# Optimization experiments

Hardware: AMD Instinct MI355X
Metric: run time of the kernel (lower is better)

Reference implementation:

```python
import jax, jax.numpy as jnp
import numpy as np

ALPHA = 0.5
E_MINUS_1 = float(np.e - 1.0)  # exp(1) - 1; exp(0) - 1 == 0

B = 4096
CLASSES = [128, 512, 2048, 8192]


def _ce(logits, labels):
    # mean cross-entropy: -mean(log_softmax(logits)[i, labels[i]])
    logp = jax.nn.log_softmax(logits, axis=-1)
    nll = -jnp.take_along_axis(logp, labels[:, None], axis=-1)[:, 0]
    return jnp.mean(nll)


def setup_inputs() -> dict:
    key = jax.random.key(0)
    ks = jax.random.split(key, 12)
    inp = {}
    for l, c in enumerate(CLASSES):
        inp[f"out{l}"] = jax.random.normal(ks[l], (B, c), dtype=jnp.float32)
    # targets[:, l] must be < CLASSES[l]; keep all < min(CLASSES) for simplicity
    inp["targets"] = jax.random.randint(ks[4], (B, 4), 0, 128).astype(jnp.int64)
    for l, c in enumerate(CLASSES):
        inp[f"pred{l}"] = jax.random.randint(ks[5 + l], (B,), 0, c).astype(jnp.int64)
    inp["valid01"] = jax.random.randint(ks[9], (128, 512), 0, 2).astype(bool)
    inp["valid12"] = jax.random.randint(ks[10], (512, 2048), 0, 2).astype(bool)
    inp["valid23"] = jax.random.randint(ks[11], (2048, 8192), 0, 2).astype(bool)
    return inp


def reference(out0, out1, out2, out3, targets, pred0, pred1, pred2, pred3,
              valid01, valid12, valid23):
    outputs = [out0, out1, out2, out3]
    preds = [pred0, pred1, pred2, pred3]
    valids = [valid01, valid12, valid23]

    total_ce = sum(_ce(outputs[l], targets[:, l]) for l in range(len(outputs)))

    # dependency loss: per sample, exp(D)-1 with D=0 if (prev_pred -> curr_pred)
    # is a valid parent-child pair, else D=1; averaged over batch, summed over levels
    total_dep = jnp.zeros((), dtype=out0.dtype)
    for l, V in enumerate(valids):
        ok = V[preds[l], preds[l + 1]]  # [B] bool gather (vectorized dict lookup)
        total_dep = total_dep + E_MINUS_1 * jnp.mean(1.0 - ok.astype(out0.dtype))

    total = ALPHA * total_ce + (1.0 - ALPHA) * total_dep
    return (total, total_ce, total_dep)
```

## Files before the change

### kernel.cpp

```cpp
#include <hip/hip_runtime.h>
#include <float.h>


#define NB 4096

static constexpr float LOG2E = 1.4426950408889634f;
static constexpr float LN2   = 0.6931471805599453f;
static constexpr float E_M1  = 1.7182818284590452f;

__device__ __forceinline__ void combine_ms(float& m, float& s, float m2, float s2) {
    float mn = fmaxf(m, m2);
    s = s * exp2f((m - mn) * LOG2E) + s2 * exp2f((m2 - mn) * LOG2E);
    m = mn;
}

__global__ __launch_bounds__(256) void ce_rows_kernel(
    const float* __restrict__ o0, const float* __restrict__ o1,
    const float* __restrict__ o2, const float* __restrict__ o3,
    const int* __restrict__ targets, float* __restrict__ nll)
{
    const int bid = blockIdx.x;
    const int lvl = 3 - (bid >> 12);
    const int row = bid & (NB - 1);

    const float* base; int C;
    if      (lvl == 0) { base = o0; C = 128;  }
    else if (lvl == 1) { base = o1; C = 512;  }
    else if (lvl == 2) { base = o2; C = 2048; }
    else               { base = o3; C = 8192; }

    const float4* rowp = (const float4*)(base + (size_t)row * C);
    const int C4 = C >> 2;

    float m = -FLT_MAX, s = 0.0f;
    for (int f = threadIdx.x; f < C4; f += 256) {
        float4 v = rowp[f];
        float m4 = fmaxf(fmaxf(v.x, v.y), fmaxf(v.z, v.w));
        float mn = fmaxf(m, m4);
        s = s * exp2f((m - mn) * LOG2E)
          + exp2f((v.x - mn) * LOG2E) + exp2f((v.y - mn) * LOG2E)
          + exp2f((v.z - mn) * LOG2E) + exp2f((v.w - mn) * LOG2E);
        m = mn;
    }

    #pragma unroll
    for (int off = 32; off; off >>= 1)
        combine_ms(m, s, __shfl_xor(m, off), __shfl_xor(s, off));

    __shared__ float lm[4], ls[4];
    const int wv = threadIdx.x >> 6;
    if ((threadIdx.x & 63) == 0) { lm[wv] = m; ls[wv] = s; }
    __syncthreads();

    if (threadIdx.x == 0) {
        float M = lm[0], S = ls[0];
        #pragma unroll
        for (int w = 1; w < 4; w++) combine_ms(M, S, lm[w], ls[w]);
        const int t  = targets[row * 4 + lvl];
        const float xt = base[(size_t)row * C + t];
        nll[lvl * NB + row] = M + log2f(S) * LN2 - xt;
    }
}

__global__ __launch_bounds__(1024) void finalize_kernel(
    const float* __restrict__ nll,
    const int* __restrict__ p0, const int* __restrict__ p1,
    const int* __restrict__ p2, const int* __restrict__ p3,
    const int* __restrict__ v01, const int* __restrict__ v12,
    const int* __restrict__ v23, float* __restrict__ out)
{
    const int tid = threadIdx.x;

    float ce[4] = {0.f, 0.f, 0.f, 0.f};
    #pragma unroll
    for (int l = 0; l < 4; l++)
        for (int i = tid; i < NB; i += 1024)
            ce[l] += nll[l * NB + i];

    float ok[3] = {0.f, 0.f, 0.f};
    for (int i = tid; i < NB; i += 1024) {
        const int a = p0[i], b = p1[i], c = p2[i], d = p3[i];
        ok[0] += (v01[a * 512  + b] != 0) ? 1.f : 0.f;
        ok[1] += (v12[b * 2048 + c] != 0) ? 1.f : 0.f;
        ok[2] += (v23[c * 8192 + d] != 0) ? 1.f : 0.f;
    }

    __shared__ float lds[16];
    float vals[7] = {ce[0], ce[1], ce[2], ce[3], ok[0], ok[1], ok[2]};
    float res[7];
    #pragma unroll
    for (int q = 0; q < 7; q++) {
        float v = vals[q];
        #pragma unroll
        for (int off = 32; off; off >>= 1) v += __shfl_xor(v, off);
        if ((tid & 63) == 0) lds[tid >> 6] = v;
        __syncthreads();
        if (tid == 0) {
            float t = 0.f;
            #pragma unroll
            for (int w = 0; w < 16; w++) t += lds[w];
            res[q] = t;
        }
        __syncthreads();
    }

    if (tid == 0) {
        const float inv_b = 1.0f / (float)NB;
        float total_ce = (res[0] + res[1] + res[2] + res[3]) * inv_b;
        float total_dep = 0.f;
        #pragma unroll
        for (int q = 4; q < 7; q++)
            total_dep += E_M1 * (((float)NB - res[q]) * inv_b);
        out[0] = 0.5f * total_ce + 0.5f * total_dep;
        out[1] = total_ce;
        out[2] = total_dep;
    }
}

extern "C" void kernel_launch(void* const* d_in, const int* in_sizes, int n_in,
                              void* d_out, int out_size, void* d_ws, size_t ws_size,
                              hipStream_t stream)
{
    const float* o0 = (const float*)d_in[0];
    const float* o1 = (const float*)d_in[1];
    const float* o2 = (const float*)d_in[2];
    const float* o3 = (const float*)d_in[3];
    const int* targets = (const int*)d_in[4];
    const int* p0 = (const int*)d_in[5];
    const int* p1 = (const int*)d_in[6];
    const int* p2 = (const int*)d_in[7];
    const int* p3 = (const int*)d_in[8];
    const int* v01 = (const int*)d_in[9];
    const int* v12 = (const int*)d_in[10];
    const int* v23 = (const int*)d_in[11];

    float* nll = (float*)d_ws;
    float* out = (float*)d_out;

    ce_rows_kernel<<<4 * NB, 256, 0, stream>>>(o0, o1, o2, o3, targets, nll);
    finalize_kernel<<<1, 1024, 0, stream>>>(nll, p0, p1, p2, p3, v01, v12, v23, out);
}
```

Measured before the change: 308.2 us.

## Fuse all four CE levels per row into one block with two-pass softmax

Replaces the 4*NB per-(level,row) blocks with NB blocks that each load one row of all four logit matrices into registers up front. Each block then computes the max and sum-exp in two passes, using explicit per-wave max/sum reductions instead of the online-softmax combine. The finalize kernel now reads nll as float4 per row, batches its gathers, and does a single LDS reduction round instead of seven synchronized ones. This should cut block-launch overhead, improve memory-level parallelism and remove redundant exp rescaling, at the cost of more registers and wave-specialized branches.

Result: faster. 298.0 us (-3.3%).

```diff
diff --git a/kernel.cpp b/kernel.cpp
--- a/kernel.cpp
+++ b/kernel.cpp
@@ -8,57 +8,122 @@
 static constexpr float LN2   = 0.6931471805599453f;
 static constexpr float E_M1  = 1.7182818284590452f;
 
-__device__ __forceinline__ void combine_ms(float& m, float& s, float m2, float s2) {
-    float mn = fmaxf(m, m2);
-    s = s * exp2f((m - mn) * LOG2E) + s2 * exp2f((m2 - mn) * LOG2E);
-    m = mn;
-}
-
-__global__ __launch_bounds__(256) void ce_rows_kernel(
+__device__ __forceinline__ float wave_max(float v) {
+    #pragma unroll
+    for (int off = 32; off; off >>= 1) v = fmaxf(v, __shfl_xor(v, off));
+    return v;
+}
+__device__ __forceinline__ float wave_sum(float v) {
+    #pragma unroll
+    for (int off = 32; off; off >>= 1) v += __shfl_xor(v, off);
+    return v;
+}
+__device__ __forceinline__ float max4(float4 v) {
+    return fmaxf(fmaxf(v.x, v.y), fmaxf(v.z, v.w));
+}
+__device__ __forceinline__ float sumexp4(float4 v, float M) {
+    return exp2f((v.x - M) * LOG2E) + exp2f((v.y - M) * LOG2E)
+         + exp2f((v.z - M) * LOG2E) + exp2f((v.w - M) * LOG2E);
+}
+
+__global__ __launch_bounds__(256) void ce_fused_kernel(
     const float* __restrict__ o0, const float* __restrict__ o1,
     const float* __restrict__ o2, const float* __restrict__ o3,
     const int* __restrict__ targets, float* __restrict__ nll)
 {
-    const int bid = blockIdx.x;
-    const int lvl = 3 - (bid >> 12);
-    const int row = bid & (NB - 1);
-
-    const float* base; int C;
-    if      (lvl == 0) { base = o0; C = 128;  }
-    else if (lvl == 1) { base = o1; C = 512;  }
-    else if (lvl == 2) { base = o2; C = 2048; }
-    else               { base = o3; C = 8192; }
-
-    const float4* rowp = (const float4*)(base + (size_t)row * C);
-    const int C4 = C >> 2;
-
-    float m = -FLT_MAX, s = 0.0f;
-    for (int f = threadIdx.x; f < C4; f += 256) {
-        float4 v = rowp[f];
-        float m4 = fmaxf(fmaxf(v.x, v.y), fmaxf(v.z, v.w));
-        float mn = fmaxf(m, m4);
-        s = s * exp2f((m - mn) * LOG2E)
-          + exp2f((v.x - mn) * LOG2E) + exp2f((v.y - mn) * LOG2E)
-          + exp2f((v.z - mn) * LOG2E) + exp2f((v.w - mn) * LOG2E);
-        m = mn;
-    }
-
-    #pragma unroll
-    for (int off = 32; off; off >>= 1)
-        combine_ms(m, s, __shfl_xor(m, off), __shfl_xor(s, off));
-
-    __shared__ float lm[4], ls[4];
-    const int wv = threadIdx.x >> 6;
-    if ((threadIdx.x & 63) == 0) { lm[wv] = m; ls[wv] = s; }
+    const int row  = blockIdx.x;
+    const int tid  = threadIdx.x;
+    const int wv   = tid >> 6;
+    const int lane = tid & 63;
+
+    const float4* r3 = (const float4*)(o3 + (size_t)row * 8192);
+    float4 v3[8];
+    #pragma unroll
+    for (int k = 0; k < 8; k++) v3[k] = r3[tid + (k << 8)];
+
+    const float4* r0 = (const float4*)(o0 + (size_t)row * 128);
+    const float4* r1 = (const float4*)(o1 + (size_t)row * 512);
+    const float4* r2 = (const float4*)(o2 + (size_t)row * 2048);
+    float4 vs[4];
+    if (wv == 0) {
+        if (lane < 32) vs[0] = r0[lane];
+    } else if (wv == 1) {
+        vs[0] = r1[lane];
+        vs[1] = r1[lane + 64];
+    } else {
+        const int t2 = tid - 128;
+        #pragma unroll
+        for (int j = 0; j < 4; j++) vs[j] = r2[t2 + j * 128];
+    }
+
+    float xt_a = 0.0f, xt_b = 0.0f;
+    if (tid == 0) {
+        xt_a = o3[(size_t)row * 8192 + targets[row * 4 + 3]];
+        xt_b = o0[(size_t)row * 128  + targets[row * 4 + 0]];
+    } else if (tid == 64) {
+        xt_a = o1[(size_t)row * 512  + targets[row * 4 + 1]];
+    } else if (tid == 128) {
+        xt_a = o2[(size_t)row * 2048 + targets[row * 4 + 2]];
+    }
+
+    __shared__ float lm3[4], lm2[2], ls3[4], ls2[2];
+
+    float m3 = -FLT_MAX;
+    #pragma unroll
+    for (int k = 0; k < 8; k++) m3 = fmaxf(m3, max4(v3[k]));
+    m3 = wave_max(m3);
+
+    float msml = -FLT_MAX;
+    if (wv == 0) {
+        if (lane < 32) msml = max4(vs[0]);
+    } else if (wv == 1) {
+        msml = fmaxf(max4(vs[0]), max4(vs[1]));
+    } else {
+        #pragma unroll
+        for (int j = 0; j < 4; j++) msml = fmaxf(msml, max4(vs[j]));
+    }
+    msml = wave_max(msml);
+
+    if (lane == 0) {
+        lm3[wv] = m3;
+        if (wv >= 2) lm2[wv - 2] = msml;
+    }
     __syncthreads();
 
-    if (threadIdx.x == 0) {
-        float M = lm[0], S = ls[0];
-        #pragma unroll
-        for (int w = 1; w < 4; w++) combine_ms(M, S, lm[w], ls[w]);
-        const int t  = targets[row * 4 + lvl];
-        const float xt = base[(size_t)row * C + t];
-        nll[lvl * NB + row] = M + log2f(S) * LN2 - xt;
+    const float M3 = fmaxf(fmaxf(lm3[0], lm3[1]), fmaxf(lm3[2], lm3[3]));
+    const float M2 = (wv >= 2) ? fmaxf(lm2[0], lm2[1]) : 0.0f;
+
+    float s3 = 0.0f;
+    #pragma unroll
+    for (int k = 0; k < 8; k++) s3 += sumexp4(v3[k], M3);
+    s3 = wave_sum(s3);
+
+    float ssml = 0.0f;
+    if (wv == 0) {
+        if (lane < 32) ssml = sumexp4(vs[0], msml);
+    } else if (wv == 1) {
+        ssml = sumexp4(vs[0], msml) + sumexp4(vs[1], msml);
+    } else {
+        #pragma unroll
+        for (int j = 0; j < 4; j++) ssml += sumexp4(vs[j], M2);
+    }
+    ssml = wave_sum(ssml);
+
+    if (lane == 0) {
+        ls3[wv] = s3;
+        if (wv >= 2) ls2[wv - 2] = ssml;
+    }
+    __syncthreads();
+
+    if (tid == 0) {
+        const float S3 = ls3[0] + ls3[1] + ls3[2] + ls3[3];
+        nll[row * 4 + 3] = M3 + log2f(S3) * LN2 - xt_a;
+        nll[row * 4 + 0] = msml + log2f(ssml) * LN2 - xt_b;
+    } else if (tid == 64) {
+        nll[row * 4 + 1] = msml + log2f(ssml) * LN2 - xt_a;
+    } else if (tid == 128) {
+        const float S2 = ls2[0] + ls2[1];
+        nll[row * 4 + 2] = M2 + log2f(S2) * LN2 - xt_a;
     }
 }
 
@@ -71,42 +136,51 @@
 {
     const int tid = threadIdx.x;
 
-    float ce[4] = {0.f, 0.f, 0.f, 0.f};
-    #pragma unroll
-    for (int l = 0; l < 4; l++)
-        for (int i = tid; i < NB; i += 1024)
-            ce[l] += nll[l * NB + i];
-
-    float ok[3] = {0.f, 0.f, 0.f};
-    for (int i = tid; i < NB; i += 1024) {
-        const int a = p0[i], b = p1[i], c = p2[i], d = p3[i];
-        ok[0] += (v01[a * 512  + b] != 0) ? 1.f : 0.f;
-        ok[1] += (v12[b * 2048 + c] != 0) ? 1.f : 0.f;
-        ok[2] += (v23[c * 8192 + d] != 0) ? 1.f : 0.f;
-    }
-
-    __shared__ float lds[16];
-    float vals[7] = {ce[0], ce[1], ce[2], ce[3], ok[0], ok[1], ok[2]};
-    float res[7];
+    const float4* nr = (const float4*)nll;
+    float c0 = 0.f, c1 = 0.f, c2 = 0.f, c3 = 0.f;
+    #pragma unroll
+    for (int j = 0; j < 4; j++) {
+        float4 v = nr[tid + j * 1024];
+        c0 += v.x; c1 += v.y; c2 += v.z; c3 += v.w;
+    }
+
+    int a[4], b[4], c[4], d[4];
+    #pragma unroll
+    for (int j = 0; j < 4; j++) {
+        const int i = tid + j * 1024;
+        a[j] = p0[i]; b[j] = p1[i]; c[j] = p2[i]; d[j] = p3[i];
+    }
+    float ok0 = 0.f, ok1 = 0.f, ok2 = 0.f;
+    #pragma unroll
+    for (int j = 0; j < 4; j++) {
+        ok0 += (v01[a[j] * 512  + b[j]] != 0) ? 1.f : 0.f;
+        ok1 += (v12[b[j] * 2048 + c[j]] != 0) ? 1.f : 0.f;
+        ok2 += (v23[c[j] * 8192 + d[j]] != 0) ? 1.f : 0.f;
+    }
+
+    float vals[7] = {c0, c1, c2, c3, ok0, ok1, ok2};
     #pragma unroll
     for (int q = 0; q < 7; q++) {
-        float v = vals[q];
-        #pragma unroll
-        for (int off = 32; off; off >>= 1) v += __shfl_xor(v, off);
-        if ((tid & 63) == 0) lds[tid >> 6] = v;
-        __syncthreads();
-        if (tid == 0) {
+        #pragma unroll
+        for (int off = 32; off; off >>= 1) vals[q] += __shfl_xor(vals[q], off);
+    }
+    __shared__ float lds[16][7];
+    if ((tid & 63) == 0) {
+        #pragma unroll
+        for (int q = 0; q < 7; q++) lds[tid >> 6][q] = vals[q];
+    }
+    __syncthreads();
+
+    if (tid == 0) {
+        float res[7];
+        #pragma unroll
+        for (int q = 0; q < 7; q++) {
             float t = 0.f;
-            #pragma unroll
-            for (int w = 0; w < 16; w++) t += lds[w];
+            for (int w = 0; w < 16; w++) t += lds[w][q];
             res[q] = t;
         }
-        __syncthreads();
-    }
-
-    if (tid == 0) {
         const float inv_b = 1.0f / (float)NB;
-        float total_ce = (res[0] + res[1] + res[2] + res[3]) * inv_b;
+        const float total_ce = (res[0] + res[1] + res[2] + res[3]) * inv_b;
         float total_dep = 0.f;
         #pragma unroll
         for (int q = 4; q < 7; q++)
@@ -137,6 +211,6 @@
     float* nll = (float*)d_ws;
     float* out = (float*)d_out;
 
-    ce_rows_kernel<<<4 * NB, 256, 0, stream>>>(o0, o1, o2, o3, targets, nll);
+    ce_fused_kernel<<<NB, 256, 0, stream>>>(o0, o1, o2, o3, targets, nll);
     finalize_kernel<<<1, 1024, 0, stream>>>(nll, p0, p1, p2, p3, v01, v12, v23, out);
 }
```
